# Optimization experiments

Measured on AMD Instinct MI355X. Metric: run time of the kernel, lower is better.

The kernel has to match this reference:

```python
import jax, jax.numpy as jnp
import numpy as np

DIM = 768
NUM_HEADS = 12
POLY_DEG = 3
GRID = (24, 24)
BATCH = 16


def _make_powers():
    H, W = GRID
    ii, jj = np.meshgrid(np.arange(H), np.arange(W), indexing='ij')
    coords = np.stack([ii.ravel(), jj.ravel()], axis=-1).astype(np.float32)  # [HW, 2]
    dists = np.abs(coords[:, None, :] - coords[None, :, :]).sum(-1)  # L1 cdist [HW, HW]
    powers = np.stack([dists ** i for i in range(POLY_DEG + 1)], axis=0)  # [deg+1, HW, HW]
    return jnp.asarray(powers, dtype=jnp.float32)


def setup_inputs() -> dict:
    key = jax.random.key(0)
    ks = jax.random.split(key, 5)
    N = GRID[0] * GRID[1] + 1  # 577
    x = jax.random.normal(ks[0], (BATCH, N, DIM), dtype=jnp.float32)
    # nn.Linear weights stored as [in, out] for direct matmul; qkv_bias=False
    W_qkv = jax.random.normal(ks[1], (DIM, 3 * DIM), dtype=jnp.float32) * (DIM ** -0.5)
    W_proj = jax.random.normal(ks[2], (DIM, DIM), dtype=jnp.float32) * (DIM ** -0.5)
    b_proj = jnp.zeros((DIM,), dtype=jnp.float32)
    # small scale keeps polynomial bias (distances up to 46, cubed) numerically sane
    poly_coeffs = jax.random.normal(ks[3], (NUM_HEADS, POLY_DEG + 1), dtype=jnp.float32) * 0.01
    powers = _make_powers()
    return {"x": x, "W_qkv": W_qkv, "W_proj": W_proj, "b_proj": b_proj,
            "poly_coeffs": poly_coeffs, "powers": powers}


def reference(x, W_qkv, W_proj, b_proj, poly_coeffs, powers):
    B, N, C = x.shape
    h = NUM_HEADS
    d = C // h
    scale = d ** -0.5
    qkv = (x @ W_qkv).reshape(B, N, 3, h, d)
    qkv = jnp.transpose(qkv, (2, 0, 3, 1, 4))  # [3, B, h, N, d]
    q, k, v = qkv[0], qkv[1], qkv[2]
    # polynomial relative-position bias, padded with zeros for CLS row/col
    rpe = jnp.einsum('hd,dxy->hxy', poly_coeffs, powers)  # [h, HW, HW]
    rpe = jnp.pad(rpe, ((0, 0), (1, 0), (1, 0)))  # [h, N, N]
    attn = scale * jnp.einsum('bhnd,bhmd->bhnm', q, k) + rpe[None]
    attn = jax.nn.softmax(attn, axis=-1)
    out = jnp.einsum('bhnm,bhmd->bhnd', attn, v)
    out = jnp.transpose(out, (0, 2, 1, 3)).reshape(B, N, C)
    return out @ W_proj + b_proj
```

## Files before the change

### kernel.cpp

```cpp
#include <hip/hip_runtime.h>


using u16 = unsigned short;
using u32 = unsigned int;

typedef __bf16 bf16x8 __attribute__((ext_vector_type(8)));
typedef float f32x4 __attribute__((ext_vector_type(4)));

__device__ inline u16 f2bf(float f) {
    u32 u = __builtin_bit_cast(u32, f);
    u32 r = u + 0x7fffu + ((u >> 16) & 1u);
    return (u16)(r >> 16);
}
__device__ inline float bf2f(u16 x) {
    return __builtin_bit_cast(float, (u32)x << 16);
}

__device__ inline f32x4 mfma16(bf16x8 a, bf16x8 b, f32x4 c) {
    return __builtin_amdgcn_mfma_f32_16x16x32_bf16(a, b, c, 0, 0, 0);
}

__device__ inline float fexp2(float x) { return __builtin_amdgcn_exp2f(x); }

__device__ inline int xcd_remap(int bid, int nwg) {
    const int q = nwg >> 3, r = nwg & 7;
    const int xcd = bid & 7, idx = bid >> 3;
    return (xcd < r ? xcd * (q + 1) : r * (q + 1) + (xcd - r) * q) + idx;
}

__device__ inline float dpp_max16(float v) {
    int x;
    x = __builtin_amdgcn_update_dpp(0, __builtin_bit_cast(int, v), 0xB1, 0xF, 0xF, true);
    v = fmaxf(v, __builtin_bit_cast(float, x));
    x = __builtin_amdgcn_update_dpp(0, __builtin_bit_cast(int, v), 0x4E, 0xF, 0xF, true);
    v = fmaxf(v, __builtin_bit_cast(float, x));
    x = __builtin_amdgcn_update_dpp(0, __builtin_bit_cast(int, v), 0x124, 0xF, 0xF, true);
    v = fmaxf(v, __builtin_bit_cast(float, x));
    x = __builtin_amdgcn_update_dpp(0, __builtin_bit_cast(int, v), 0x128, 0xF, 0xF, true);
    v = fmaxf(v, __builtin_bit_cast(float, x));
    return v;
}

#define GLOAD_LDS16(g, l)                                                          \
    __builtin_amdgcn_global_load_lds((const __attribute__((address_space(1))) u32*)(g), \
                                     (__attribute__((address_space(3))) u32*)(l), 16, 0, 0)

#define BAR()    asm volatile("s_barrier" ::: "memory")
#define WAITV8() asm volatile("s_waitcnt vmcnt(8)" ::: "memory")
#define WAITV4() asm volatile("s_waitcnt vmcnt(4)" ::: "memory")
#define WAITV0() asm volatile("s_waitcnt vmcnt(0)" ::: "memory")

__global__ void k_prep(const float* __restrict__ x, const float* __restrict__ Wq,
                       const float* __restrict__ Wp, u16* __restrict__ xb,
                       u16* __restrict__ wqkv, u16* __restrict__ wprj) {
    const int bid = blockIdx.x;
    const int t = threadIdx.x;
    if (bid < 576) {
        __shared__ float tile[64][65];
        const float* src;
        u16* dst;
        int C, rt, ct;
        if (bid < 432) { src = Wq; dst = wqkv; C = 2304; rt = bid / 36; ct = bid % 36; }
        else { const int b2 = bid - 432; src = Wp; dst = wprj; C = 768; rt = b2 / 12; ct = b2 % 12; }
        const int row0 = rt * 64, col0 = ct * 64;
#pragma unroll
        for (int it = 0; it < 4; ++it) {
            const int row = it * 16 + (t >> 4);
            const float4 v = *(const float4*)&src[(size_t)(row0 + row) * C + col0 + (t & 15) * 4];
            tile[row][(t & 15) * 4 + 0] = v.x;
            tile[row][(t & 15) * 4 + 1] = v.y;
            tile[row][(t & 15) * 4 + 2] = v.z;
            tile[row][(t & 15) * 4 + 3] = v.w;
        }
        __syncthreads();
#pragma unroll
        for (int it = 0; it < 4; ++it) {
            const int oc = it * 16 + (t >> 4);
            const int orr = (t & 15) * 4;
            ushort4 o;
            o.x = f2bf(tile[orr + 0][oc]);
            o.y = f2bf(tile[orr + 1][oc]);
            o.z = f2bf(tile[orr + 2][oc]);
            o.w = f2bf(tile[orr + 3][oc]);
            *(ushort4*)&dst[(size_t)(col0 + oc) * 768 + row0 + orr] = o;
        }
    } else {
        const int n4 = 9232 * 768 / 4;
        const int stride = (2048 - 576) * 256;
        for (int i = (bid - 576) * 256 + t; i < n4; i += stride) {
            float4 v = ((const float4*)x)[i];
            ushort4 o;
            o.x = f2bf(v.x); o.y = f2bf(v.y); o.z = f2bf(v.z); o.w = f2bf(v.w);
            ((ushort4*)xb)[i] = o;
        }
    }
}

__device__ inline void stageAB(const u16* __restrict__ Ag, const u16* __restrict__ Bg,
                               u16* L, int t) {
#pragma unroll
    for (int c = 0; c < 2; ++c) {
        const int p = c * 256 + t;
        const int row = p >> 2, ch = p & 3;
        const int src = row * 768 + ((ch ^ ((row >> 1) & 3)) * 8);
        GLOAD_LDS16(Ag + src, L + p * 8);
        GLOAD_LDS16(Bg + src, L + 4096 + p * 8);
    }
}
__device__ inline bf16x8 ldfrag32(const u16* base, int row, int slot) {
    return *(const bf16x8*)(base + row * 32 + ((slot ^ ((row >> 1) & 3)) * 8));
}

template <int MODE, int NB>
__launch_bounds__(256, 2)
__global__ void k_gemm(const u16* __restrict__ A, const u16* __restrict__ Bw,
                       u16* __restrict__ q_out, u16* __restrict__ k_out,
                       u16* __restrict__ v_out,
                       float* __restrict__ f_out, const float* __restrict__ bias) {
    constexpr int NT = 24;
    constexpr int M = 9232;
    const int wgid = xcd_remap(blockIdx.x, gridDim.x);
    const int mbase = (wgid / NB) * 128;
    const int nbase = (wgid - (wgid / NB) * NB) * 128;
    __shared__ alignas(16) u16 lds[4][8192];
    const int t = threadIdx.x;
    const int lane = t & 63, w = t >> 6;
    const int lr = lane & 15, lg = lane >> 4;
    const int wrow = (w >> 1) * 64, wcol = (w & 1) * 64;
    const u16* Ag = A + (size_t)mbase * 768;
    const u16* Bg = Bw + (size_t)nbase * 768;
    f32x4 acc[4][4] = {};

    stageAB(Ag, Bg, &lds[0][0], t);
    stageAB(Ag + 32, Bg + 32, &lds[1][0], t);
    stageAB(Ag + 64, Bg + 64, &lds[2][0], t);
    WAITV8();
    BAR();

    for (int kt = 0; kt < NT; ++kt) {
        const u16* Lc = &lds[kt & 3][0];
        if (kt + 3 < NT)
            stageAB(Ag + (kt + 3) * 32, Bg + (kt + 3) * 32, &lds[(kt + 3) & 3][0], t);
        bf16x8 af[4], bv[4];
#pragma unroll
        for (int i = 0; i < 4; ++i)
            af[i] = ldfrag32(Lc, wrow + i * 16 + lr, lg);
#pragma unroll
        for (int j = 0; j < 4; ++j)
            bv[j] = ldfrag32(Lc + 4096, wcol + j * 16 + lr, lg);
        __builtin_amdgcn_s_setprio(1);
#pragma unroll
        for (int i = 0; i < 4; ++i)
#pragma unroll
            for (int j = 0; j < 4; ++j)
                acc[i][j] = mfma16(af[i], bv[j], acc[i][j]);
        __builtin_amdgcn_s_setprio(0);
        if (kt + 1 < NT) {
            if (kt < NT - 3)       { WAITV8(); }
            else if (kt == NT - 3) { WAITV4(); }
            else                   { WAITV0(); }
            BAR();
        }
    }

#pragma unroll
    for (int i = 0; i < 4; ++i) {
#pragma unroll
        for (int j = 0; j < 4; ++j) {
            const int col = nbase + wcol + j * 16 + lr;
#pragma unroll
            for (int r = 0; r < 4; ++r) {
                const int row = mbase + wrow + i * 16 + 4 * lg + r;
                if (row < M) {
                    if (MODE == 0) {
                        const int bb = row / 577;
                        const int nn = row - bb * 577;
                        const int tt = col / 768;
                        const int rem = col - tt * 768;
                        const int hh = rem >> 6, dd = rem & 63;
                        const size_t bh = (size_t)bb * 12 + hh;
                        const u16 val = f2bf(acc[i][j][r]);
                        if (tt == 0)      q_out[(bh * 640 + nn) * 64 + dd] = val;
                        else if (tt == 1) k_out[(bh * 640 + nn) * 64 + dd] = val;
                        else              v_out[(bh * 64 + dd) * 640 + nn] = val;
                    } else {
                        f_out[(size_t)row * 768 + col] = acc[i][j][r] + bias[col];
                    }
                }
            }
        }
    }
}

__launch_bounds__(256, 2)
__global__ void k_attn(const u16* __restrict__ Qg, const u16* __restrict__ Kg,
                       const u16* __restrict__ Vtg, const float* __restrict__ coef,
                       u16* __restrict__ Og) {
    const int wgid = xcd_remap(blockIdx.x, gridDim.x);
    const int bh = wgid / 5;
    const int qt = wgid - bh * 5;
    const int b = bh / 12, h = bh - b * 12;
    const int t = threadIdx.x;
    const int lane = t & 63, w = t >> 6;
    const int lr = lane & 15, lg = lane >> 4;
    __shared__ alignas(16) u16 Kl[2][8192];
    __shared__ alignas(16) u16 Vl[2][8192];

    const float l2e = 1.4426950408889634f;
    const float hc0 = coef[h * 4 + 0] * l2e, hc1 = coef[h * 4 + 1] * l2e,
                hc2 = coef[h * 4 + 2] * l2e, hc3 = coef[h * 4 + 3] * l2e;

    bf16x8 onesv;
#pragma unroll
    for (int j = 0; j < 8; ++j) onesv[j] = (__bf16)1.0f;

    const int qrow0 = qt * 128 + w * 32;
    bf16x8 qa[2][2];
#pragma unroll
    for (int i = 0; i < 2; ++i) {
        const u16* qp = Qg + ((size_t)bh * 640 + qrow0 + i * 16 + lr) * 64;
        qa[i][0] = *(const bf16x8*)(qp + lg * 8);
        qa[i][1] = *(const bf16x8*)(qp + 32 + lg * 8);
    }

    float gi[2][4], gj[2][4], nvf[2][4];
#pragma unroll
    for (int i = 0; i < 2; ++i)
#pragma unroll
        for (int r = 0; r < 4; ++r) {
            const int n = qrow0 + i * 16 + 4 * lg + r;
            nvf[i][r] = (n == 0) ? 0.f : 1.f;
            const int nm1 = (n > 0) ? n - 1 : 0;
            const int qi = nm1 / 24;
            gi[i][r] = (float)qi;
            gj[i][r] = (float)(nm1 - qi * 24);
        }

    float M[2][4];
    f32x4 Lac[2] = {};
#pragma unroll
    for (int i = 0; i < 2; ++i)
#pragma unroll
        for (int r = 0; r < 4; ++r) M[i][r] = -3e38f;
    f32x4 acco[2][4] = {};
    const float scale2 = 0.125f * 1.4426950408889634f;
    const int ch0 = ((lg ^ (lr & 7))) * 8;

    const u16* Ksb = Kg + (size_t)bh * 640 * 64;
    const u16* Vsb = Vtg + (size_t)bh * 64 * 640;
    const int krow = 32 * w + (lane >> 1), kch0 = (lane & 1) * 4;
    const int vrow = 16 * w + (lane >> 2), vch0 = (lane & 3) * 4;

    {
#pragma unroll
        for (int q = 0; q < 4; ++q) {
            uint4 kv = *(const uint4*)(Ksb + (size_t)krow * 64 + (kch0 + q) * 8);
            *(uint4*)(&Kl[0][krow * 64 + (((kch0 + q) ^ (krow & 7)) * 8)]) = kv;
            uint4 vv = *(const uint4*)(Vsb + (size_t)vrow * 640 + (vch0 + q) * 8);
            *(uint4*)(&Vl[0][vrow * 128 + (((vch0 + q) ^ (vrow & 15)) * 8)]) = vv;
        }
    }
    __syncthreads();
    int cur = 0;

    for (int kt = 0; kt < 4; ++kt) {
        const u16* Kc = &Kl[cur][0];
        const u16* Vc = &Vl[cur][0];
        u16* pb0 = &Kl[cur ^ 1][32 * w * 64];
        u16* pb1 = &Vl[cur ^ 1][16 * w * 128];

        f32x4 sac[2][8];
        __builtin_amdgcn_s_setprio(1);
#pragma unroll
        for (int cb = 0; cb < 8; ++cb) {
            const int row = cb * 16 + lr;
            const bf16x8 kb0 = *(const bf16x8*)(Kc + row * 64 + ch0);
            const bf16x8 kb1 = *(const bf16x8*)(Kc + row * 64 + (ch0 ^ 32));
#pragma unroll
            for (int i = 0; i < 2; ++i) {
                f32x4 z = {};
                z = mfma16(qa[i][0], kb0, z);
                sac[i][cb] = mfma16(qa[i][1], kb1, z);
            }
        }
        __builtin_amdgcn_s_setprio(0);

        float tm[2][4];
#pragma unroll
        for (int i = 0; i < 2; ++i)
#pragma unroll
            for (int r = 0; r < 4; ++r) tm[i][r] = -3e38f;
#pragma unroll
        for (int cb = 0; cb < 8; ++cb) {
            const int m = kt * 128 + cb * 16 + lr;
            const float mvf = (m == 0) ? 0.f : 1.f;
            const int mm1 = (m > 0) ? m - 1 : 0;
            const int pi = mm1 / 24;
            const float ci = (float)pi;
            const float cj = (float)(mm1 - pi * 24);
#pragma unroll
            for (int i = 0; i < 2; ++i)
#pragma unroll
                for (int r = 0; r < 4; ++r) {
                    const float d = fabsf(gi[i][r] - ci) + fabsf(gj[i][r] - cj);
                    float rp = fmaf(hc3, d, hc2);
                    rp = fmaf(rp, d, hc1);
                    rp = fmaf(rp, d, hc0);
                    const float v = fmaf(sac[i][cb][r], scale2,
                                         rp * (mvf * nvf[i][r]));
                    sac[i][cb][r] = v;
                    tm[i][r] = fmaxf(tm[i][r], v);
                }
        }
#pragma unroll
        for (int i = 0; i < 2; ++i)
#pragma unroll
            for (int r = 0; r < 4; ++r) tm[i][r] = dpp_max16(tm[i][r]);

        float over = -3e38f;
#pragma unroll
        for (int i = 0; i < 2; ++i)
#pragma unroll
            for (int r = 0; r < 4; ++r) over = fmaxf(over, tm[i][r] - M[i][r]);
        if (__any(over > 11.5f)) {
#pragma unroll
            for (int i = 0; i < 2; ++i)
#pragma unroll
                for (int r = 0; r < 4; ++r) {
                    const float Mn = fmaxf(M[i][r], tm[i][r]);
                    const float a = fexp2(M[i][r] - Mn);
                    Lac[i][r] *= a;
                    acco[i][0][r] *= a; acco[i][1][r] *= a;
                    acco[i][2][r] *= a; acco[i][3][r] *= a;
                    M[i][r] = Mn;
                }
        }

#pragma unroll
        for (int i = 0; i < 2; ++i) {
            u16* pb = i ? pb1 : pb0;
#pragma unroll
            for (int cb = 0; cb < 8; ++cb)
#pragma unroll
                for (int r = 0; r < 4; ++r) {
                    const float p = fexp2(sac[i][cb][r] - M[i][r]);
                    const int rw = 4 * lg + r;
                    pb[rw * 128 + (((2 * cb + (lr >> 3)) ^ (rw & 15)) * 8) + (lr & 7)] =
                        (u16)(__builtin_bit_cast(u32, p) >> 16);
                }
        }

        uint4 nk[4], nv[4];
        {
            const u16* Ks = Ksb + (size_t)(kt + 1) * 128 * 64;
            const u16* Vs = Vsb + (size_t)(kt + 1) * 128;
#pragma unroll
            for (int q = 0; q < 4; ++q) {
                nk[q] = *(const uint4*)(Ks + (size_t)krow * 64 + (kch0 + q) * 8);
                nv[q] = *(const uint4*)(Vs + (size_t)vrow * 640 + (vch0 + q) * 8);
            }
        }

        __builtin_amdgcn_s_setprio(1);
#pragma unroll
        for (int s = 0; s < 4; ++s) {
            const bf16x8 pa0 = *(const bf16x8*)(pb0 + lr * 128 + (((4 * s + lg) ^ (lr & 15)) * 8));
            const bf16x8 pa1 = *(const bf16x8*)(pb1 + lr * 128 + (((4 * s + lg) ^ (lr & 15)) * 8));
            Lac[0] = mfma16(pa0, onesv, Lac[0]);
            Lac[1] = mfma16(pa1, onesv, Lac[1]);
#pragma unroll
            for (int f = 0; f < 4; ++f) {
                const int vr = f * 16 + lr;
                const bf16x8 vb = *(const bf16x8*)(Vc + vr * 128 + (((4 * s + lg) ^ (vr & 15)) * 8));
                acco[0][f] = mfma16(pa0, vb, acco[0][f]);
                acco[1][f] = mfma16(pa1, vb, acco[1][f]);
            }
        }
        __builtin_amdgcn_s_setprio(0);

#pragma unroll
        for (int q = 0; q < 4; ++q) {
            *(uint4*)(&Kl[cur ^ 1][krow * 64 + (((kch0 + q) ^ (krow & 7)) * 8)]) = nk[q];
            *(uint4*)(&Vl[cur ^ 1][vrow * 128 + (((vch0 + q) ^ (vrow & 15)) * 8)]) = nv[q];
        }
        __syncthreads();
        cur ^= 1;
    }

    {
        const u16* Kc = &Kl[cur][0];
        const u16* Vc = &Vl[cur][0];
        u16* pb0 = &Kl[cur ^ 1][32 * w * 64];
        u16* pb1 = &Vl[cur ^ 1][16 * w * 128];

        f32x4 sac[2][5];
        __builtin_amdgcn_s_setprio(1);
#pragma unroll
        for (int cb = 0; cb < 5; ++cb) {
            const int row = cb * 16 + lr;
            const bf16x8 kb0 = *(const bf16x8*)(Kc + row * 64 + ch0);
            const bf16x8 kb1 = *(const bf16x8*)(Kc + row * 64 + (ch0 ^ 32));
#pragma unroll
            for (int i = 0; i < 2; ++i) {
                f32x4 z = {};
                z = mfma16(qa[i][0], kb0, z);
                sac[i][cb] = mfma16(qa[i][1], kb1, z);
            }
        }
        __builtin_amdgcn_s_setprio(0);

        float tm[2][4];
#pragma unroll
        for (int i = 0; i < 2; ++i)
#pragma unroll
            for (int r = 0; r < 4; ++r) tm[i][r] = -3e38f;
#pragma unroll
        for (int cb = 0; cb < 5; ++cb) {
            const int m = 512 + cb * 16 + lr;
            const bool valid = (m <= 576);
            const int mm1 = m - 1;
            const int pi = mm1 / 24;
            const float ci = (float)((pi < 24) ? pi : 23);
            const float cj = (float)((pi < 24) ? (mm1 - pi * 24) : 23);
#pragma unroll
            for (int i = 0; i < 2; ++i)
#pragma unroll
                for (int r = 0; r < 4; ++r) {
                    const float d = fabsf(gi[i][r] - ci) + fabsf(gj[i][r] - cj);
                    float rp = fmaf(hc3, d, hc2);
                    rp = fmaf(rp, d, hc1);
                    rp = fmaf(rp, d, hc0);
                    float v = fmaf(sac[i][cb][r], scale2, rp * nvf[i][r]);
                    v = valid ? v : -1e30f;
                    sac[i][cb][r] = v;
                    tm[i][r] = fmaxf(tm[i][r], v);
                }
        }
#pragma unroll
        for (int i = 0; i < 2; ++i)
#pragma unroll
            for (int r = 0; r < 4; ++r) tm[i][r] = dpp_max16(tm[i][r]);

        float over = -3e38f;
#pragma unroll
        for (int i = 0; i < 2; ++i)
#pragma unroll
            for (int r = 0; r < 4; ++r) over = fmaxf(over, tm[i][r] - M[i][r]);
        if (__any(over > 11.5f)) {
#pragma unroll
            for (int i = 0; i < 2; ++i)
#pragma unroll
                for (int r = 0; r < 4; ++r) {
                    const float Mn = fmaxf(M[i][r], tm[i][r]);
                    const float a = fexp2(M[i][r] - Mn);
                    Lac[i][r] *= a;
                    acco[i][0][r] *= a; acco[i][1][r] *= a;
                    acco[i][2][r] *= a; acco[i][3][r] *= a;
                    M[i][r] = Mn;
                }
        }

#pragma unroll
        for (int i = 0; i < 2; ++i) {
            u16* pb = i ? pb1 : pb0;
#pragma unroll
            for (int cb = 0; cb < 5; ++cb)
#pragma unroll
                for (int r = 0; r < 4; ++r) {
                    const float p = fexp2(sac[i][cb][r] - M[i][r]);
                    const int rw = 4 * lg + r;
                    pb[rw * 128 + (((2 * cb + (lr >> 3)) ^ (rw & 15)) * 8) + (lr & 7)] =
                        (u16)(__builtin_bit_cast(u32, p) >> 16);
                }
#pragma unroll
            for (int r = 0; r < 4; ++r) {
                const int rw = 4 * lg + r;
                pb[rw * 128 + (((10 + (lr >> 3)) ^ (rw & 15)) * 8) + (lr & 7)] = 0;
            }
        }

        __builtin_amdgcn_s_setprio(1);
#pragma unroll
        for (int s = 0; s < 3; ++s) {
            const bf16x8 pa0 = *(const bf16x8*)(pb0 + lr * 128 + (((4 * s + lg) ^ (lr & 15)) * 8));
            const bf16x8 pa1 = *(const bf16x8*)(pb1 + lr * 128 + (((4 * s + lg) ^ (lr & 15)) * 8));
            Lac[0] = mfma16(pa0, onesv, Lac[0]);
            Lac[1] = mfma16(pa1, onesv, Lac[1]);
#pragma unroll
            for (int f = 0; f < 4; ++f) {
                const int vr = f * 16 + lr;
                const bf16x8 vb = *(const bf16x8*)(Vc + vr * 128 + (((4 * s + lg) ^ (vr & 15)) * 8));
                acco[0][f] = mfma16(pa0, vb, acco[0][f]);
                acco[1][f] = mfma16(pa1, vb, acco[1][f]);
            }
        }
        __builtin_amdgcn_s_setprio(0);
    }

#pragma unroll
    for (int i = 0; i < 2; ++i)
#pragma unroll
        for (int r = 0; r < 4; ++r) {
            const float inv = __builtin_amdgcn_rcpf(Lac[i][r]);
            const int n = qrow0 + i * 16 + 4 * lg + r;
            if (n < 577) {
#pragma unroll
                for (int f = 0; f < 4; ++f)
                    Og[((size_t)b * 577 + n) * 768 + h * 64 + f * 16 + lr] =
                        f2bf(acco[i][f][r] * inv);
            }
        }
}

extern "C" void kernel_launch(void* const* d_in, const int* in_sizes, int n_in,
                              void* d_out, int out_size, void* d_ws, size_t ws_size,
                              hipStream_t stream) {
    const float* x      = (const float*)d_in[0];
    const float* W_qkv  = (const float*)d_in[1];
    const float* W_proj = (const float*)d_in[2];
    const float* b_proj = (const float*)d_in[3];
    const float* coef   = (const float*)d_in[4];
    float* out = (float*)d_out;
    char* ws = (char*)d_ws;

    u16* xb   = (u16*)(ws + 0);
    u16* Og   = (u16*)(ws + 0);
    u16* wqkv = (u16*)(ws + 14180352);
    u16* wprj = (u16*)(ws + 17719296);
    u16* Qg   = (u16*)(ws + 18898944);
    u16* Kg   = (u16*)(ws + 34627584);
    u16* Vtg  = (u16*)(ws + 50356224);

    k_prep<<<2048, 256, 0, stream>>>(x, W_qkv, W_proj, xb, wqkv, wprj);

    k_gemm<0, 18><<<18 * 73, 256, 0, stream>>>(xb, wqkv, Qg, Kg, Vtg,
                                               nullptr, nullptr);
    k_attn<<<960, 256, 0, stream>>>(Qg, Kg, Vtg, coef, Og);
    k_gemm<1, 6><<<6 * 73, 256, 0, stream>>>(Og, wprj, nullptr, nullptr,
                                             nullptr, out, b_proj);
}
```

Before: 157.4 us.

## Enlarge GEMM tiles to 256x256 with 512 threads and split-phase pipelining

Replaces the 128x128, 256-thread GEMM with a 256x256 tile computed by 8 waves. It uses 128 KB of dynamic LDS and a 4-buffer, 3-deep prefetch that interleaves A and B stage loads between two halves of the MFMA work. The aim is higher arithmetic intensity per byte loaded and fewer redundant global reads for both the QKV and output projections. In exchange there are far fewer workgroups (333 and 111) on a 256-CU device, so the projection GEMM cannot fill the machine. The large LDS footprint also limits each CU to one workgroup.

```diff
diff --git a/kernel.cpp b/kernel.cpp
--- a/kernel.cpp
+++ b/kernel.cpp
@@ -96,81 +96,93 @@
     }
 }
 
-__device__ inline void stageAB(const u16* __restrict__ Ag, const u16* __restrict__ Bg,
-                               u16* L, int t) {
-#pragma unroll
-    for (int c = 0; c < 2; ++c) {
-        const int p = c * 256 + t;
-        const int row = p >> 2, ch = p & 3;
-        const int src = row * 768 + ((ch ^ ((row >> 1) & 3)) * 8);
-        GLOAD_LDS16(Ag + src, L + p * 8);
-        GLOAD_LDS16(Bg + src, L + 4096 + p * 8);
-    }
-}
-__device__ inline bf16x8 ldfrag32(const u16* base, int row, int slot) {
-    return *(const bf16x8*)(base + row * 32 + ((slot ^ ((row >> 1) & 3)) * 8));
-}
-
 template <int MODE, int NB>
-__launch_bounds__(256, 2)
-__global__ void k_gemm(const u16* __restrict__ A, const u16* __restrict__ Bw,
-                       u16* __restrict__ q_out, u16* __restrict__ k_out,
-                       u16* __restrict__ v_out,
-                       float* __restrict__ f_out, const float* __restrict__ bias) {
-    constexpr int NT = 24;
+__launch_bounds__(512, 2)
+__global__ void k_gemm2(const u16* __restrict__ A, const u16* __restrict__ Bw,
+                        u16* __restrict__ q_out, u16* __restrict__ k_out,
+                        u16* __restrict__ v_out,
+                        float* __restrict__ f_out, const float* __restrict__ bias) {
     constexpr int M = 9232;
+    extern __shared__ u16 lds[];
     const int wgid = xcd_remap(blockIdx.x, gridDim.x);
-    const int mbase = (wgid / NB) * 128;
-    const int nbase = (wgid - (wgid / NB) * NB) * 128;
-    __shared__ alignas(16) u16 lds[4][8192];
-    const int t = threadIdx.x;
-    const int lane = t & 63, w = t >> 6;
+    const int mbase = (wgid / NB) * 256;
+    const int nbase = (wgid - (wgid / NB) * NB) * 256;
+    const int tid = threadIdx.x;
+    const int lane = tid & 63, w = tid >> 6;
     const int lr = lane & 15, lg = lane >> 4;
-    const int wrow = (w >> 1) * 64, wcol = (w & 1) * 64;
+    const int wm = w >> 2, wn = w & 3;
     const u16* Ag = A + (size_t)mbase * 768;
     const u16* Bg = Bw + (size_t)nbase * 768;
-    f32x4 acc[4][4] = {};
-
-    stageAB(Ag, Bg, &lds[0][0], t);
-    stageAB(Ag + 32, Bg + 32, &lds[1][0], t);
-    stageAB(Ag + 64, Bg + 64, &lds[2][0], t);
+    f32x4 acc[8][4] = {};
+
+    auto stage2 = [&](int H, int part) {
+        const int koff = (H >> 1) * 64 + (H & 1) * 32;
+        const u16* G = part ? Bg : Ag;
+        u16* D = lds + (part ? 32768 : 0) + (H & 3) * 8192;
+#pragma unroll
+        for (int l = 0; l < 2; ++l) {
+            const int p = l * 512 + tid;
+            const int row = p >> 2, chp = p & 3;
+            GLOAD_LDS16(G + (size_t)row * 768 + koff + ((chp ^ ((row >> 1) & 3)) * 8),
+                        D + p * 8);
+        }
+    };
+    auto ldfrag = [&](const u16* base, int row) {
+        return *(const bf16x8*)(base + row * 32 + ((lg ^ ((row >> 1) & 3)) * 8));
+    };
+
+    stage2(0, 0); stage2(0, 1);
+    stage2(1, 0); stage2(1, 1);
+    stage2(2, 0); stage2(2, 1);
     WAITV8();
     BAR();
 
-    for (int kt = 0; kt < NT; ++kt) {
-        const u16* Lc = &lds[kt & 3][0];
-        if (kt + 3 < NT)
-            stageAB(Ag + (kt + 3) * 32, Bg + (kt + 3) * 32, &lds[(kt + 3) & 3][0], t);
-        bf16x8 af[4], bv[4];
-#pragma unroll
-        for (int i = 0; i < 4; ++i)
-            af[i] = ldfrag32(Lc, wrow + i * 16 + lr, lg);
-#pragma unroll
-        for (int j = 0; j < 4; ++j)
-            bv[j] = ldfrag32(Lc + 4096, wcol + j * 16 + lr, lg);
+    for (int H = 0; H < 24; ++H) {
+        const u16* Ah = lds + (H & 3) * 8192;
+        const u16* Bh = lds + 32768 + (H & 3) * 8192;
+        const bool pre = (H + 3) < 24;
+        bf16x8 bv[4], af[4];
+#pragma unroll
+        for (int n = 0; n < 4; ++n) bv[n] = ldfrag(Bh, wn * 64 + n * 16 + lr);
+#pragma unroll
+        for (int m = 0; m < 4; ++m) af[m] = ldfrag(Ah, wm * 128 + m * 16 + lr);
+        if (pre) stage2(H + 3, 0);
+        BAR();
         __builtin_amdgcn_s_setprio(1);
 #pragma unroll
-        for (int i = 0; i < 4; ++i)
-#pragma unroll
-            for (int j = 0; j < 4; ++j)
-                acc[i][j] = mfma16(af[i], bv[j], acc[i][j]);
+        for (int m = 0; m < 4; ++m)
+#pragma unroll
+            for (int n = 0; n < 4; ++n)
+                acc[m][n] = mfma16(af[m], bv[n], acc[m][n]);
         __builtin_amdgcn_s_setprio(0);
-        if (kt + 1 < NT) {
-            if (kt < NT - 3)       { WAITV8(); }
-            else if (kt == NT - 3) { WAITV4(); }
-            else                   { WAITV0(); }
-            BAR();
-        }
-    }
-
-#pragma unroll
-    for (int i = 0; i < 4; ++i) {
-#pragma unroll
-        for (int j = 0; j < 4; ++j) {
-            const int col = nbase + wcol + j * 16 + lr;
+        BAR();
+#pragma unroll
+        for (int m = 0; m < 4; ++m) af[m] = ldfrag(Ah, wm * 128 + (m + 4) * 16 + lr);
+        if (pre) stage2(H + 3, 1);
+        BAR();
+        __builtin_amdgcn_s_setprio(1);
+#pragma unroll
+        for (int m = 0; m < 4; ++m)
+#pragma unroll
+            for (int n = 0; n < 4; ++n)
+                acc[m + 4][n] = mfma16(af[m], bv[n], acc[m + 4][n]);
+        __builtin_amdgcn_s_setprio(0);
+        if (H < 23) {
+            if (H <= 20)      { WAITV8(); }
+            else if (H == 21) { WAITV4(); }
+            else              { WAITV0(); }
+        }
+        BAR();
+    }
+
+#pragma unroll
+    for (int m = 0; m < 8; ++m) {
+#pragma unroll
+        for (int n = 0; n < 4; ++n) {
+            const int col = nbase + wn * 64 + n * 16 + lr;
 #pragma unroll
             for (int r = 0; r < 4; ++r) {
-                const int row = mbase + wrow + i * 16 + 4 * lg + r;
+                const int row = mbase + wm * 128 + m * 16 + 4 * lg + r;
                 if (row < M) {
                     if (MODE == 0) {
                         const int bb = row / 577;
@@ -179,12 +191,12 @@
                         const int rem = col - tt * 768;
                         const int hh = rem >> 6, dd = rem & 63;
                         const size_t bh = (size_t)bb * 12 + hh;
-                        const u16 val = f2bf(acc[i][j][r]);
+                        const u16 val = f2bf(acc[m][n][r]);
                         if (tt == 0)      q_out[(bh * 640 + nn) * 64 + dd] = val;
                         else if (tt == 1) k_out[(bh * 640 + nn) * 64 + dd] = val;
                         else              v_out[(bh * 64 + dd) * 640 + nn] = val;
                     } else {
-                        f_out[(size_t)row * 768 + col] = acc[i][j][r] + bias[col];
+                        f_out[(size_t)row * 768 + col] = acc[m][n][r] + bias[col];
                     }
                 }
             }
@@ -533,9 +545,9 @@
 
     k_prep<<<2048, 256, 0, stream>>>(x, W_qkv, W_proj, xb, wqkv, wprj);
 
-    k_gemm<0, 18><<<18 * 73, 256, 0, stream>>>(xb, wqkv, Qg, Kg, Vtg,
-                                               nullptr, nullptr);
+    k_gemm2<0, 9><<<37 * 9, 512, 131072, stream>>>(xb, wqkv, Qg, Kg, Vtg,
+                                                   nullptr, nullptr);
     k_attn<<<960, 256, 0, stream>>>(Qg, Kg, Vtg, coef, Og);
-    k_gemm<1, 6><<<6 * 73, 256, 0, stream>>>(Og, wprj, nullptr, nullptr,
-                                             nullptr, out, b_proj);
-}
+    k_gemm2<1, 3><<<37 * 3, 512, 131072, stream>>>(Og, wprj, nullptr, nullptr,
+                                                   nullptr, out, b_proj);
+}
```

New measurement: 190.7 us. +21.2%, slower.
